# Kernel optimization log

Hardware: AMD Instinct MI355X
Metric: run time of the kernel (lower is better)

Reference implementation:

```python
import jax, jax.numpy as jnp
import numpy as np

DIM, D_STATE, D_CONV, EXPAND = 384, 16, 4, 2
D_INNER = EXPAND * DIM          # 768
DT_RANK = -(-DIM // 16)         # 24
B_, T_, H_, W_ = 2, 8, 16, 16
EPS = 1e-5


def layernorm(x, w, b):
    mu = x.mean(-1, keepdims=True)
    var = ((x - mu) ** 2).mean(-1, keepdims=True)
    return (x - mu) * jax.lax.rsqrt(var + EPS) * w + b


def setup_inputs() -> dict:
    key = jax.random.key(0)
    ks = jax.random.split(key, 12)
    std = 0.02
    x = jax.random.normal(ks[0], (B_, DIM, T_, H_, W_), jnp.float32)
    params = dict(
        ln1_w=jnp.ones((DIM,), jnp.float32),
        ln1_b=jnp.zeros((DIM,), jnp.float32),
        ln2_w=jnp.ones((DIM,), jnp.float32),
        ln2_b=jnp.zeros((DIM,), jnp.float32),
        in_proj_w=std * jax.random.normal(ks[1], (2 * D_INNER, DIM), jnp.float32),
        conv_w=std * jax.random.normal(ks[2], (D_INNER, 1, D_CONV), jnp.float32),
        conv_b=jnp.zeros((D_INNER,), jnp.float32),
        x_proj_w=std * jax.random.normal(ks[3], (DT_RANK + 2 * D_STATE, D_INNER), jnp.float32),
        dt_proj_w=std * jax.random.normal(ks[4], (D_INNER, DT_RANK), jnp.float32),
        dt_proj_b=0.01 * jax.random.normal(ks[5], (D_INNER,), jnp.float32),
        A_log=jnp.log(jnp.broadcast_to(jnp.arange(1, D_STATE + 1, dtype=jnp.float32), (D_INNER, D_STATE))),
        D=jnp.ones((D_INNER,), jnp.float32),
        out_proj_w=std * jax.random.normal(ks[6], (DIM, D_INNER), jnp.float32),
    )
    return {"x": x, **params}


def mamba(xn, in_proj_w, conv_w, conv_b, x_proj_w, dt_proj_w, dt_proj_b, A_log, D, out_proj_w):
    # xn: [B, L, dim]
    B, L, _ = xn.shape
    xz = xn @ in_proj_w.T                      # [B, L, 2*d_inner]
    u, z = jnp.split(xz, 2, axis=-1)
    # causal depthwise conv over tokens
    uc = jnp.transpose(u, (0, 2, 1))           # [B, d_inner, L]
    uc = jax.lax.conv_general_dilated(
        uc, conv_w, window_strides=(1,), padding=[(D_CONV - 1, 0)],
        dimension_numbers=("NCH", "OIH", "NCH"), feature_group_count=D_INNER)
    u = jax.nn.silu(jnp.transpose(uc, (0, 2, 1)) + conv_b)  # [B, L, d_inner]

    dbc = u @ x_proj_w.T                       # [B, L, dt_rank + 2*d_state]
    dt = dbc[..., :DT_RANK]
    Bm = dbc[..., DT_RANK:DT_RANK + D_STATE]   # [B, L, d_state]
    Cm = dbc[..., DT_RANK + D_STATE:]          # [B, L, d_state]
    delta = jax.nn.softplus(dt @ dt_proj_w.T + dt_proj_b)   # [B, L, d_inner]

    A = -jnp.exp(A_log)                        # [d_inner, d_state]
    deltaA = jnp.exp(delta[..., None] * A)                     # [B, L, d_inner, d_state]
    deltaBu = delta[..., None] * Bm[:, :, None, :] * u[..., None]

    def step(h, inp):
        dA, dBu, c = inp                       # [B,d_inner,d_state], [B,d_inner,d_state], [B,d_state]
        h = dA * h + dBu
        y = jnp.einsum("bds,bs->bd", h, c)
        return h, y

    h0 = jnp.zeros((B, D_INNER, D_STATE), xn.dtype)
    xs = (jnp.moveaxis(deltaA, 1, 0), jnp.moveaxis(deltaBu, 1, 0), jnp.moveaxis(Cm, 1, 0))
    _, ys = jax.lax.scan(step, h0, xs)
    y = jnp.moveaxis(ys, 0, 1)                 # [B, L, d_inner]
    y = y + u * D
    y = y * jax.nn.silu(z)
    return y @ out_proj_w.T                    # [B, L, dim]


def reference(x, ln1_w, ln1_b, ln2_w, ln2_b, in_proj_w, conv_w, conv_b,
              x_proj_w, dt_proj_w, dt_proj_b, A_log, D, out_proj_w):
    B, C, T, H, W = x.shape
    L = T * H * W
    x_flat = jnp.transpose(x.reshape(B, C, L), (0, 2, 1))   # [B, L, C]
    x_norm = layernorm(x_flat, ln1_w, ln1_b)
    x_mamba = mamba(x_norm, in_proj_w, conv_w, conv_b, x_proj_w,
                    dt_proj_w, dt_proj_b, A_log, D, out_proj_w)
    x_out = layernorm(x_flat + x_mamba, ln2_w, ln2_b)
    return jnp.transpose(x_out, (0, 2, 1)).reshape(B, C, T, H, W)
```

## Files before the change

### kernel.cpp

```cpp
#include <hip/hip_runtime.h>
#include <hip/hip_bf16.h>

typedef unsigned short u16;
typedef unsigned int   u32;
typedef __attribute__((ext_vector_type(8))) short short8;
typedef __attribute__((ext_vector_type(4))) float f32x4;

#define B_   2
#define L_   2048
#define CDIM 384
#define DI   768
#define DXZ  1536
#define DTR  24
#define DS   16
#define NDBC 56
#define NC   64
#define TC   32
#define TL   32
#define EPSV 1e-5f

#define OFFW_WIN  0
#define OFFW_WXP  589824
#define OFFW_WOUT 632832
#define TOTW      927744

__device__ __forceinline__ float bf2f(u16 u) {
    union { u32 i; float f; } v; v.i = ((u32)u) << 16; return v.f;
}
__device__ __forceinline__ u16 f2bf(float f) {
    union { float f; u32 i; } v; v.f = f;
    u32 x = v.i;
    u32 r = (x + 0x7FFFu + ((x >> 16) & 1u)) >> 16;
    return (u16)r;
}

__global__ __launch_bounds__(256) void ln1_convert(const float* __restrict__ x,
                                                   const float* __restrict__ w,
                                                   const float* __restrict__ bb,
                                                   u16* __restrict__ xn,
                                                   const float* __restrict__ win,
                                                   const float* __restrict__ wxp,
                                                   const float* __restrict__ wout,
                                                   u16* __restrict__ wdst) {
    __shared__ float tile[CDIM][TL + 1];
    __shared__ float red_s[8][TL];
    __shared__ float red_s2[8][TL];
    __shared__ float mu_s[TL], rs_s[TL];
    int tid = threadIdx.x, blk = blockIdx.x;
    if (blk >= 128) {
        int base = (blk - 128) * 256 + tid;
        for (int e = base; e < TOTW; e += 128 * 256) {
            float v;
            if (e < OFFW_WXP)       v = win[e];
            else if (e < OFFW_WOUT) v = wxp[e - OFFW_WXP];
            else                    v = wout[e - OFFW_WOUT];
            wdst[e] = f2bf(v);
        }
        return;
    }
    int b = blk >> 6;
    int l0 = (blk & 63) * TL;
    int cg = tid >> 5, li = tid & 31;
    const float* xp = x + (size_t)b * CDIM * L_ + l0 + li;
    float s = 0.f, s2 = 0.f;
#pragma unroll
    for (int c = cg; c < CDIM; c += 8) {
        float v = xp[(size_t)c * L_];
        tile[c][li] = v;
        s += v; s2 += v * v;
    }
    red_s[cg][li] = s; red_s2[cg][li] = s2;
    __syncthreads();
    if (tid < TL) {
        float ts = 0.f, ts2 = 0.f;
#pragma unroll
        for (int g = 0; g < 8; g++) { ts += red_s[g][tid]; ts2 += red_s2[g][tid]; }
        float mu = ts / CDIM;
        float var = ts2 / CDIM - mu * mu;
        mu_s[tid] = mu; rs_s[tid] = rsqrtf(var + EPSV);
    }
    __syncthreads();
    int wv = tid >> 6, lane = tid & 63;
#pragma unroll
    for (int r = 0; r < 8; r++) {
        int l = wv * 8 + r;
        float mu = mu_s[l], rs = rs_s[l];
        u16* op = xn + (size_t)(b * L_ + l0 + l) * CDIM;
#pragma unroll
        for (int j = 0; j < 6; j++) {
            int c = lane + 64 * j;
            float t = (tile[c][l] - mu) * rs * w[c] + bb[c];
            op[c] = f2bf(t);
        }
    }
}

template<int KN>
__global__ __launch_bounds__(256) void gemm_in(const u16* __restrict__ A,
                                               const u16* __restrict__ Bm,
                                               u16* __restrict__ Cp, int Nn) {
    int wave = threadIdx.x >> 6, lane = threadIdx.x & 63;
    int wm = wave & 1, wn = wave >> 1;
    int m0 = (blockIdx.x * 2 + wm) * 64;
    int n0 = (blockIdx.y * 2 + wn) * 64;
    int r = lane & 15, q = lane >> 4;
    f32x4 acc[4][4];
#pragma unroll
    for (int i = 0; i < 4; i++)
#pragma unroll
        for (int j = 0; j < 4; j++)
#pragma unroll
            for (int g = 0; g < 4; g++) acc[i][j][g] = 0.f;
#pragma unroll
    for (int k0 = 0; k0 < KN; k0 += 32) {
        short8 af[4], bf[4];
        int ka = k0 + q * 8;
#pragma unroll
        for (int i = 0; i < 4; i++) {
            af[i] = *(const short8*)(A + (size_t)(m0 + i * 16 + r) * KN + ka);
            bf[i] = *(const short8*)(Bm + (size_t)(n0 + i * 16 + r) * KN + ka);
        }
#pragma unroll
        for (int i = 0; i < 4; i++)
#pragma unroll
            for (int j = 0; j < 4; j++)
                acc[i][j] = __builtin_amdgcn_mfma_f32_16x16x32_bf16(af[i], bf[j], acc[i][j], 0, 0, 0);
    }
#pragma unroll
    for (int i = 0; i < 4; i++)
#pragma unroll
        for (int j = 0; j < 4; j++) {
            int col = n0 + j * 16 + r;
#pragma unroll
            for (int g = 0; g < 4; g++)
                Cp[(size_t)(m0 + i * 16 + q * 4 + g) * Nn + col] = f2bf(acc[i][j][g]);
        }
}

template<int KN, int NN>
__global__ __launch_bounds__(256) void gemm_out(const u16* __restrict__ A,
                                                const u16* __restrict__ Bm,
                                                float* __restrict__ Cp) {
    __shared__ float sm[2][64][66];
    int lane = threadIdx.x & 63, wave = threadIdx.x >> 6;
    int m0 = blockIdx.x * 64, n0 = blockIdx.y * 64;
    int r = lane & 15, q = lane >> 4;
    f32x4 acc[4][4];
#pragma unroll
    for (int i = 0; i < 4; i++)
#pragma unroll
        for (int j = 0; j < 4; j++)
#pragma unroll
            for (int g = 0; g < 4; g++) acc[i][j][g] = 0.f;
    const int KQ = KN / 4;
    int kb = wave * KQ;
#pragma unroll
    for (int k0 = 0; k0 < KQ; k0 += 32) {
        short8 af[4], bf[4];
        int ka = kb + k0 + q * 8;
#pragma unroll
        for (int i = 0; i < 4; i++) {
            af[i] = *(const short8*)(A + (size_t)(m0 + i * 16 + r) * KN + ka);
            bf[i] = *(const short8*)(Bm + (size_t)(n0 + i * 16 + r) * KN + ka);
        }
#pragma unroll
        for (int i = 0; i < 4; i++)
#pragma unroll
            for (int j = 0; j < 4; j++)
                acc[i][j] = __builtin_amdgcn_mfma_f32_16x16x32_bf16(af[i], bf[j], acc[i][j], 0, 0, 0);
    }
    if (wave < 2) {
#pragma unroll
        for (int i = 0; i < 4; i++)
#pragma unroll
            for (int j = 0; j < 4; j++)
#pragma unroll
                for (int g = 0; g < 4; g++)
                    sm[wave][i * 16 + q * 4 + g][j * 16 + r] = acc[i][j][g];
    }
    __syncthreads();
    if (wave >= 2) {
        int w2 = wave - 2;
#pragma unroll
        for (int i = 0; i < 4; i++)
#pragma unroll
            for (int j = 0; j < 4; j++)
#pragma unroll
                for (int g = 0; g < 4; g++)
                    sm[w2][i * 16 + q * 4 + g][j * 16 + r] += acc[i][j][g];
    }
    __syncthreads();
    for (int e = threadIdx.x; e < 64 * 64; e += 256) {
        int row = e >> 6, col = e & 63;
        Cp[(size_t)(m0 + row) * NN + n0 + col] = sm[0][row][col] + sm[1][row][col];
    }
}

template<int KN>
__global__ __launch_bounds__(256) void gemm_xp(const u16* __restrict__ A,
                                               const u16* __restrict__ Bm,
                                               float* __restrict__ Cp) {
    __shared__ float sm[2][16][66];
    int lane = threadIdx.x & 63, wave = threadIdx.x >> 6;
    int m0 = blockIdx.x * 16;
    int r = lane & 15, q = lane >> 4;
    f32x4 acc[4];
#pragma unroll
    for (int j = 0; j < 4; j++)
#pragma unroll
        for (int g = 0; g < 4; g++) acc[j][g] = 0.f;
    short8 zf;
#pragma unroll
    for (int e = 0; e < 8; e++) zf[e] = 0;
    const int KQ = KN / 4;
    int kb = wave * KQ;
#pragma unroll
    for (int k0 = 0; k0 < KQ; k0 += 32) {
        int ka = kb + k0 + q * 8;
        short8 af = *(const short8*)(A + (size_t)(m0 + r) * KN + ka);
        short8 bf[4];
#pragma unroll
        for (int j = 0; j < 4; j++) {
            int n = j * 16 + r;
            bf[j] = (n < NDBC) ? *(const short8*)(Bm + (size_t)n * KN + ka) : zf;
        }
#pragma unroll
        for (int j = 0; j < 4; j++)
            acc[j] = __builtin_amdgcn_mfma_f32_16x16x32_bf16(af, bf[j], acc[j], 0, 0, 0);
    }
    if (wave < 2) {
#pragma unroll
        for (int j = 0; j < 4; j++)
#pragma unroll
            for (int g = 0; g < 4; g++)
                sm[wave][q * 4 + g][j * 16 + r] = acc[j][g];
    }
    __syncthreads();
    if (wave >= 2) {
        int w2 = wave - 2;
#pragma unroll
        for (int j = 0; j < 4; j++)
#pragma unroll
            for (int g = 0; g < 4; g++)
                sm[w2][q * 4 + g][j * 16 + r] += acc[j][g];
    }
    __syncthreads();
    for (int e = threadIdx.x; e < 16 * 64; e += 256) {
        int row = e >> 6, col = e & 63;
        if (col < NDBC) {
            Cp[(size_t)(m0 + row) * NDBC + col] = sm[0][row][col] + sm[1][row][col];
        }
    }
}

__global__ __launch_bounds__(256) void conv_silu(const u16* __restrict__ xz,
                                                 const float* __restrict__ cw,
                                                 const float* __restrict__ cb,
                                                 u16* __restrict__ ubf) {
    int d = blockIdx.y * 256 + threadIdx.x;
    int m0 = blockIdx.x * 16;
    int l0 = m0 & (L_ - 1);
    float4 c4 = ((const float4*)cw)[d];
    float bias = cb[d];
    float w0, w1, w2;
    if (l0 == 0) { w0 = w1 = w2 = 0.f; }
    else {
        w0 = bf2f(xz[(size_t)(m0 - 3) * DXZ + d]);
        w1 = bf2f(xz[(size_t)(m0 - 2) * DXZ + d]);
        w2 = bf2f(xz[(size_t)(m0 - 1) * DXZ + d]);
    }
#pragma unroll
    for (int i = 0; i < 16; i++) {
        int m = m0 + i;
        float cur = bf2f(xz[(size_t)m * DXZ + d]);
        float acc = bias + w0 * c4.x + w1 * c4.y + w2 * c4.z + cur * c4.w;
        float sg = 1.f / (1.f + __expf(-acc));
        ubf[(size_t)m * DI + d] = f2bf(acc * sg);
        w0 = w1; w1 = w2; w2 = cur;
    }
}

__global__ __launch_bounds__(256) void scan_pass1(const u16* __restrict__ ubf,
                                                  const float* __restrict__ dbc,
                                                  const float* __restrict__ alogf,
                                                  const float* __restrict__ wdtf,
                                                  const float* __restrict__ bdtf,
                                                  float* __restrict__ chA,
                                                  float* __restrict__ chB) {
    int bc = blockIdx.x;
    int b = bc >> 6, chunk = bc & 63;
    int d = blockIdx.y * 256 + threadIdx.x;
    float a[DS], ap[DS], bv[DS], wdt[DTR];
#pragma unroll
    for (int s = 0; s < DS; s++) { a[s] = -__expf(alogf[d * DS + s]); ap[s] = 1.f; bv[s] = 0.f; }
#pragma unroll
    for (int k = 0; k < DTR; k++) wdt[k] = wdtf[d * DTR + k];
    float bd = bdtf[d];
    int t0 = b * L_ + chunk * TC;
#pragma unroll 2
    for (int t = t0; t < t0 + TC; t++) {
        const float* row = dbc + (size_t)t * NDBC;
        float acc = bd;
#pragma unroll
        for (int k = 0; k < DTR; k++) acc += row[k] * wdt[k];
        float dd = (acc > 20.f) ? acc : __logf(1.f + __expf(acc));
        float du = dd * bf2f(ubf[(size_t)t * DI + d]);
#pragma unroll
        for (int s = 0; s < DS; s++) {
            float dA = __expf(dd * a[s]);
            bv[s] = dA * bv[s] + du * row[DTR + s];
            ap[s] *= dA;
        }
    }
    float* pa = chA + (size_t)bc * DS * DI + d;
    float* pb = chB + (size_t)bc * DS * DI + d;
#pragma unroll
    for (int s = 0; s < DS; s++) { pa[(size_t)s * DI] = ap[s]; pb[(size_t)s * DI] = bv[s]; }
}

__global__ __launch_bounds__(256) void scan_mid(const float* __restrict__ chA,
                                                const float* __restrict__ chB,
                                                float* __restrict__ hin) {
    int idx = blockIdx.x * 256 + threadIdx.x;
    int b = idx / (DI * DS);
    int rem = idx - b * (DI * DS);
    float h = 0.f;
#pragma unroll 4
    for (int c = 0; c < NC; c++) {
        size_t off = ((size_t)(b * NC + c) * DI) * DS + rem;
        hin[off] = h;
        h = chA[off] * h + chB[off];
    }
}

__global__ __launch_bounds__(256) void scan_pass2(const u16* __restrict__ ubf,
                                                  const float* __restrict__ dbc,
                                                  const float* __restrict__ alogf,
                                                  const float* __restrict__ wdtf,
                                                  const float* __restrict__ bdtf,
                                                  const float* __restrict__ hin,
                                                  const float* __restrict__ Dwf,
                                                  const u16* __restrict__ xz,
                                                  u16* __restrict__ ym) {
    int bc = blockIdx.x;
    int b = bc >> 6, chunk = bc & 63;
    int d = blockIdx.y * 256 + threadIdx.x;
    float a[DS], h[DS], wdt[DTR];
#pragma unroll
    for (int s = 0; s < DS; s++) a[s] = -__expf(alogf[d * DS + s]);
#pragma unroll
    for (int k = 0; k < DTR; k++) wdt[k] = wdtf[d * DTR + k];
    float bd = bdtf[d];
    const float* hp = hin + (size_t)bc * DS * DI + d;
#pragma unroll
    for (int s = 0; s < DS; s++) h[s] = hp[(size_t)s * DI];
    float dD = Dwf[d];
    int t0 = b * L_ + chunk * TC;
#pragma unroll 2
    for (int t = t0; t < t0 + TC; t++) {
        const float* row = dbc + (size_t)t * NDBC;
        float acc = bd;
#pragma unroll
        for (int k = 0; k < DTR; k++) acc += row[k] * wdt[k];
        float dd = (acc > 20.f) ? acc : __logf(1.f + __expf(acc));
        float uu = bf2f(ubf[(size_t)t * DI + d]);
        float du = dd * uu;
        float y = 0.f;
#pragma unroll
        for (int s = 0; s < DS; s++) {
            float dA = __expf(dd * a[s]);
            h[s] = dA * h[s] + du * row[DTR + s];
            y += h[s] * row[DTR + DS + s];
        }
        float z = bf2f(xz[(size_t)t * DXZ + DI + d]);
        float sg = 1.f / (1.f + __expf(-z));
        ym[(size_t)t * DI + d] = f2bf((y + uu * dD) * (z * sg));
    }
}

__global__ __launch_bounds__(256) void ln2_out(const float* __restrict__ x,
                                               const float* __restrict__ om,
                                               const float* __restrict__ w,
                                               const float* __restrict__ bb,
                                               float* __restrict__ out) {
    __shared__ float tile[CDIM][TL + 1];
    __shared__ float mu_s[TL], rs_s[TL];
    int tid = threadIdx.x, blk = blockIdx.x;
    int b = blk >> 6;
    int l0 = (blk & 63) * TL;
    int cg = tid >> 5, li = tid & 31;
    const float* xp = x + (size_t)b * CDIM * L_ + l0 + li;
#pragma unroll
    for (int c = cg; c < CDIM; c += 8) tile[c][li] = xp[(size_t)c * L_];
    __syncthreads();
    int wv = tid >> 6, lane = tid & 63;
#pragma unroll
    for (int r = 0; r < 8; r++) {
        int l = wv * 8 + r;
        const float* op = om + (size_t)(b * L_ + l0 + l) * CDIM;
        float s = 0.f, s2 = 0.f;
#pragma unroll
        for (int j = 0; j < 6; j++) {
            int c = lane + 64 * j;
            float t = tile[c][l] + op[c];
            tile[c][l] = t;
            s += t; s2 += t * t;
        }
#pragma unroll
        for (int off = 32; off > 0; off >>= 1) { s += __shfl_xor(s, off); s2 += __shfl_xor(s2, off); }
        if (lane == 0) {
            float mu = s / CDIM;
            float var = s2 / CDIM - mu * mu;
            mu_s[l] = mu; rs_s[l] = rsqrtf(var + EPSV);
        }
    }
    __syncthreads();
    float* outp = out + (size_t)b * CDIM * L_ + l0 + li;
    float mu = mu_s[li], rs = rs_s[li];
#pragma unroll
    for (int c = cg; c < CDIM; c += 8) {
        float t = (tile[c][li] - mu) * rs * w[c] + bb[c];
        outp[(size_t)c * L_] = t;
    }
}

extern "C" void kernel_launch(void* const* d_in, const int* in_sizes, int n_in,
                              void* d_out, int out_size, void* d_ws, size_t ws_size,
                              hipStream_t stream) {
    const float* x    = (const float*)d_in[0];
    const float* ln1w = (const float*)d_in[1];
    const float* ln1b = (const float*)d_in[2];
    const float* ln2w = (const float*)d_in[3];
    const float* ln2b = (const float*)d_in[4];
    const float* win  = (const float*)d_in[5];
    const float* cw   = (const float*)d_in[6];
    const float* cb   = (const float*)d_in[7];
    const float* wxp  = (const float*)d_in[8];
    const float* wdt  = (const float*)d_in[9];
    const float* bdt  = (const float*)d_in[10];
    const float* alog = (const float*)d_in[11];
    const float* Dw   = (const float*)d_in[12];
    const float* wout = (const float*)d_in[13];

    char* ws = (char*)d_ws;
    u16*   wbf   = (u16*)(ws + 0);
    u16*   win_b  = wbf + OFFW_WIN;
    u16*   wxp_b  = wbf + OFFW_WXP;
    u16*   wout_b = wbf + OFFW_WOUT;
    u16*   xn    = (u16*)(ws + 1855488);
    u16*   xz    = (u16*)(ws + 5001216);
    u16*   ubf   = (u16*)(ws + 17584128);
    float* dbc   = (float*)(ws + 23875584);
    float* chA   = (float*)(ws + 24793088);
    float* chB   = (float*)(ws + 31084544);
    float* hin   = (float*)(ws + 37376000);
    u16*   ym    = (u16*)(ws + 43667456);
    float* om    = (float*)(ws + 49958912);

    ln1_convert<<<dim3(256), 256, 0, stream>>>(x, ln1w, ln1b, xn, win, wxp, wout, wbf);
    gemm_in<384><<<dim3(32, 12), 256, 0, stream>>>(xn, win_b, xz, DXZ);
    conv_silu<<<dim3(256, 3), 256, 0, stream>>>(xz, cw, cb, ubf);
    gemm_xp<768><<<dim3(256), 256, 0, stream>>>(ubf, wxp_b, dbc);
    scan_pass1<<<dim3(128, 3), 256, 0, stream>>>(ubf, dbc, alog, wdt, bdt, chA, chB);
    scan_mid<<<96, 256, 0, stream>>>(chA, chB, hin);
    scan_pass2<<<dim3(128, 3), 256, 0, stream>>>(ubf, dbc, alog, wdt, bdt, hin, Dw, xz, ym);
    gemm_out<768, 384><<<dim3(64, 6), 256, 0, stream>>>(ym, wout_b, om);
    ln2_out<<<dim3(128), 256, 0, stream>>>(x, om, ln2w, ln2b, (float*)d_out);
}
```

Baseline: 219.7 us.

## Fuse all stages into one persistent kernel with grid-wide atomic barriers

Replaces the nine separate kernel launches with one persistent 256-block, 512-thread kernel. The stages (LN1, in-proj GEMM, conv, x-proj, scan passes, out-proj, LN2) are separated by software grid barriers built on atomics and sleep loops, with a memset to reset the barrier counters. The goal is to remove per-launch overhead and gaps between kernels. In exchange the kernel relies on all 256 blocks being co-resident to avoid deadlock, some stages now run on fewer blocks or with different work splits, and it adds barrier spin cost.

```diff
diff --git a/kernel.cpp b/kernel.cpp
--- a/kernel.cpp
+++ b/kernel.cpp
@@ -24,6 +24,9 @@
 #define OFFW_WOUT 632832
 #define TOTW      927744
 
+#define NBLK 256
+#define NTHR 512
+
 __device__ __forceinline__ float bf2f(u16 u) {
     union { u32 i; float f; } v; v.i = ((u32)u) << 16; return v.f;
 }
@@ -34,393 +37,400 @@
     return (u16)r;
 }
 
-__global__ __launch_bounds__(256) void ln1_convert(const float* __restrict__ x,
-                                                   const float* __restrict__ w,
-                                                   const float* __restrict__ bb,
-                                                   u16* __restrict__ xn,
-                                                   const float* __restrict__ win,
-                                                   const float* __restrict__ wxp,
-                                                   const float* __restrict__ wout,
-                                                   u16* __restrict__ wdst) {
-    __shared__ float tile[CDIM][TL + 1];
-    __shared__ float red_s[8][TL];
-    __shared__ float red_s2[8][TL];
-    __shared__ float mu_s[TL], rs_s[TL];
+__device__ __forceinline__ void gbar(int* bar, int slot) {
+    __syncthreads();
+    if (threadIdx.x == 0) {
+        int* p = bar + slot * 64;
+        __threadfence();
+        __hip_atomic_fetch_add(p, 1, __ATOMIC_RELEASE, __HIP_MEMORY_SCOPE_AGENT);
+        while (__hip_atomic_load(p, __ATOMIC_ACQUIRE, __HIP_MEMORY_SCOPE_AGENT) < NBLK)
+            __builtin_amdgcn_s_sleep(8);
+        __threadfence();
+    }
+    __syncthreads();
+}
+
+struct P0S { float tile[CDIM][TL + 1]; float red[16][TL]; float red2[16][TL]; float mu[TL]; float rs[TL]; };
+struct P3S { float sm[4][16][66]; };
+struct P7S { float sm[4][64][64]; };
+struct P8S { float tile[CDIM][TL + 1]; float mu[TL]; float rs[TL]; };
+
+__global__ __launch_bounds__(NTHR, 2) void mega(
+    const float* x, const float* ln1w, const float* ln1b,
+    const float* ln2w, const float* ln2b,
+    const float* win, const float* cw, const float* cb,
+    const float* wxp, const float* wdt, const float* bdt,
+    const float* alog, const float* Dw, const float* wout,
+    u16* wbf, u16* xn, u16* xz, u16* ubf,
+    float* dbc, float* chA, float* chB, float* hin,
+    u16* ym, float* om, float* out, int* bar)
+{
+    __shared__ __align__(16) char smem[65536];
     int tid = threadIdx.x, blk = blockIdx.x;
-    if (blk >= 128) {
-        int base = (blk - 128) * 256 + tid;
-        for (int e = base; e < TOTW; e += 128 * 256) {
+
+    if (blk < 128) {
+        P0S& S = *(P0S*)smem;
+        int b = blk >> 6, l0 = (blk & 63) * TL;
+        int cg = tid >> 5, li = tid & 31;
+        const float* xp = x + (size_t)b * CDIM * L_ + l0 + li;
+        float s = 0.f, s2 = 0.f;
+#pragma unroll
+        for (int c = cg; c < CDIM; c += 16) {
+            float v = xp[(size_t)c * L_];
+            S.tile[c][li] = v;
+            s += v; s2 += v * v;
+        }
+        S.red[cg][li] = s; S.red2[cg][li] = s2;
+        __syncthreads();
+        if (tid < TL) {
+            float ts = 0.f, ts2 = 0.f;
+#pragma unroll
+            for (int g = 0; g < 16; g++) { ts += S.red[g][tid]; ts2 += S.red2[g][tid]; }
+            float mu = ts / CDIM;
+            float var = ts2 / CDIM - mu * mu;
+            S.mu[tid] = mu; S.rs[tid] = rsqrtf(var + EPSV);
+        }
+        __syncthreads();
+        int wv = tid >> 6, lane = tid & 63;
+#pragma unroll
+        for (int r = 0; r < 4; r++) {
+            int l = wv * 4 + r;
+            float mu = S.mu[l], rs = S.rs[l];
+            u16* op = xn + (size_t)(b * L_ + l0 + l) * CDIM;
+#pragma unroll
+            for (int j = 0; j < 6; j++) {
+                int c = lane + 64 * j;
+                float t = (S.tile[c][l] - mu) * rs * ln1w[c] + ln1b[c];
+                op[c] = f2bf(t);
+            }
+        }
+    } else {
+        int base = (blk - 128) * NTHR + tid;
+        for (int e = base; e < TOTW; e += 128 * NTHR) {
             float v;
             if (e < OFFW_WXP)       v = win[e];
             else if (e < OFFW_WOUT) v = wxp[e - OFFW_WXP];
             else                    v = wout[e - OFFW_WOUT];
-            wdst[e] = f2bf(v);
-        }
-        return;
-    }
-    int b = blk >> 6;
-    int l0 = (blk & 63) * TL;
-    int cg = tid >> 5, li = tid & 31;
-    const float* xp = x + (size_t)b * CDIM * L_ + l0 + li;
-    float s = 0.f, s2 = 0.f;
-#pragma unroll
-    for (int c = cg; c < CDIM; c += 8) {
-        float v = xp[(size_t)c * L_];
-        tile[c][li] = v;
-        s += v; s2 += v * v;
-    }
-    red_s[cg][li] = s; red_s2[cg][li] = s2;
-    __syncthreads();
-    if (tid < TL) {
-        float ts = 0.f, ts2 = 0.f;
-#pragma unroll
-        for (int g = 0; g < 8; g++) { ts += red_s[g][tid]; ts2 += red_s2[g][tid]; }
-        float mu = ts / CDIM;
-        float var = ts2 / CDIM - mu * mu;
-        mu_s[tid] = mu; rs_s[tid] = rsqrtf(var + EPSV);
-    }
-    __syncthreads();
-    int wv = tid >> 6, lane = tid & 63;
-#pragma unroll
-    for (int r = 0; r < 8; r++) {
-        int l = wv * 8 + r;
-        float mu = mu_s[l], rs = rs_s[l];
-        u16* op = xn + (size_t)(b * L_ + l0 + l) * CDIM;
-#pragma unroll
-        for (int j = 0; j < 6; j++) {
-            int c = lane + 64 * j;
-            float t = (tile[c][l] - mu) * rs * w[c] + bb[c];
-            op[c] = f2bf(t);
-        }
-    }
-}
-
-template<int KN>
-__global__ __launch_bounds__(256) void gemm_in(const u16* __restrict__ A,
-                                               const u16* __restrict__ Bm,
-                                               u16* __restrict__ Cp, int Nn) {
-    int wave = threadIdx.x >> 6, lane = threadIdx.x & 63;
-    int wm = wave & 1, wn = wave >> 1;
-    int m0 = (blockIdx.x * 2 + wm) * 64;
-    int n0 = (blockIdx.y * 2 + wn) * 64;
-    int r = lane & 15, q = lane >> 4;
-    f32x4 acc[4][4];
-#pragma unroll
-    for (int i = 0; i < 4; i++)
+            wbf[e] = f2bf(v);
+        }
+    }
+    gbar(bar, 0);
+
+    if (blk < 192) {
+        int wave = tid >> 6, lane = tid & 63;
+        int wm = wave & 1, wn = wave >> 1;
+        int bx = blk & 31, by = blk >> 5;
+        int m0 = (bx * 2 + wm) * 64;
+        int n0 = (by * 4 + wn) * 64;
+        int r = lane & 15, q = lane >> 4;
+        const u16* Bw = wbf + OFFW_WIN;
+        f32x4 acc[4][4];
+#pragma unroll
+        for (int i = 0; i < 4; i++)
+#pragma unroll
+            for (int j = 0; j < 4; j++)
+#pragma unroll
+                for (int g = 0; g < 4; g++) acc[i][j][g] = 0.f;
+#pragma unroll
+        for (int k0 = 0; k0 < CDIM; k0 += 32) {
+            short8 af[4], bfv[4];
+            int ka = k0 + q * 8;
+#pragma unroll
+            for (int i = 0; i < 4; i++) {
+                af[i]  = *(const short8*)(xn + (size_t)(m0 + i * 16 + r) * CDIM + ka);
+                bfv[i] = *(const short8*)(Bw + (size_t)(n0 + i * 16 + r) * CDIM + ka);
+            }
+#pragma unroll
+            for (int i = 0; i < 4; i++)
+#pragma unroll
+                for (int j = 0; j < 4; j++)
+                    acc[i][j] = __builtin_amdgcn_mfma_f32_16x16x32_bf16(af[i], bfv[j], acc[i][j], 0, 0, 0);
+        }
+#pragma unroll
+        for (int i = 0; i < 4; i++)
+#pragma unroll
+            for (int j = 0; j < 4; j++) {
+                int col = n0 + j * 16 + r;
+#pragma unroll
+                for (int g = 0; g < 4; g++)
+                    xz[(size_t)(m0 + i * 16 + q * 4 + g) * DXZ + col] = f2bf(acc[i][j][g]);
+            }
+    }
+    gbar(bar, 1);
+
+    {
+#pragma unroll
+        for (int it = 0; it < 2; it++) {
+            int g = it * (NBLK * NTHR) + blk * NTHR + tid;
+            if (g < 768 * 256) {
+                int d = g % DI;
+                int m0 = (g / DI) * 16;
+                int l0 = m0 & (L_ - 1);
+                float4 c4 = ((const float4*)cw)[d];
+                float bias = cb[d];
+                float w0, w1, w2;
+                if (l0 == 0) { w0 = w1 = w2 = 0.f; }
+                else {
+                    w0 = bf2f(xz[(size_t)(m0 - 3) * DXZ + d]);
+                    w1 = bf2f(xz[(size_t)(m0 - 2) * DXZ + d]);
+                    w2 = bf2f(xz[(size_t)(m0 - 1) * DXZ + d]);
+                }
+#pragma unroll
+                for (int i = 0; i < 16; i++) {
+                    int m = m0 + i;
+                    float cur = bf2f(xz[(size_t)m * DXZ + d]);
+                    float acc = bias + w0 * c4.x + w1 * c4.y + w2 * c4.z + cur * c4.w;
+                    float sg = 1.f / (1.f + __expf(-acc));
+                    ubf[(size_t)m * DI + d] = f2bf(acc * sg);
+                    w0 = w1; w1 = w2; w2 = cur;
+                }
+            }
+        }
+    }
+    gbar(bar, 2);
+
+    {
+        P3S& S = *(P3S*)smem;
+        int wave = tid >> 6, lane = tid & 63;
+        int m0 = blk * 16;
+        int r = lane & 15, q = lane >> 4;
+        const u16* Bw = wbf + OFFW_WXP;
+        f32x4 acc[4];
 #pragma unroll
         for (int j = 0; j < 4; j++)
 #pragma unroll
-            for (int g = 0; g < 4; g++) acc[i][j][g] = 0.f;
-#pragma unroll
-    for (int k0 = 0; k0 < KN; k0 += 32) {
-        short8 af[4], bf[4];
-        int ka = k0 + q * 8;
-#pragma unroll
-        for (int i = 0; i < 4; i++) {
-            af[i] = *(const short8*)(A + (size_t)(m0 + i * 16 + r) * KN + ka);
-            bf[i] = *(const short8*)(Bm + (size_t)(n0 + i * 16 + r) * KN + ka);
-        }
-#pragma unroll
-        for (int i = 0; i < 4; i++)
+            for (int g = 0; g < 4; g++) acc[j][g] = 0.f;
+        short8 zf;
+#pragma unroll
+        for (int e = 0; e < 8; e++) zf[e] = 0;
+        int kb = wave * 96;
+#pragma unroll
+        for (int k0 = 0; k0 < 96; k0 += 32) {
+            int ka = kb + k0 + q * 8;
+            short8 af = *(const short8*)(ubf + (size_t)(m0 + r) * DI + ka);
+            short8 bfv[4];
+#pragma unroll
+            for (int j = 0; j < 4; j++) {
+                int n = j * 16 + r;
+                bfv[j] = (n < NDBC) ? *(const short8*)(Bw + (size_t)n * DI + ka) : zf;
+            }
 #pragma unroll
             for (int j = 0; j < 4; j++)
-                acc[i][j] = __builtin_amdgcn_mfma_f32_16x16x32_bf16(af[i], bf[j], acc[i][j], 0, 0, 0);
-    }
-#pragma unroll
-    for (int i = 0; i < 4; i++)
-#pragma unroll
-        for (int j = 0; j < 4; j++) {
-            int col = n0 + j * 16 + r;
-#pragma unroll
-            for (int g = 0; g < 4; g++)
-                Cp[(size_t)(m0 + i * 16 + q * 4 + g) * Nn + col] = f2bf(acc[i][j][g]);
-        }
-}
-
-template<int KN, int NN>
-__global__ __launch_bounds__(256) void gemm_out(const u16* __restrict__ A,
-                                                const u16* __restrict__ Bm,
-                                                float* __restrict__ Cp) {
-    __shared__ float sm[2][64][66];
-    int lane = threadIdx.x & 63, wave = threadIdx.x >> 6;
-    int m0 = blockIdx.x * 64, n0 = blockIdx.y * 64;
-    int r = lane & 15, q = lane >> 4;
-    f32x4 acc[4][4];
-#pragma unroll
-    for (int i = 0; i < 4; i++)
-#pragma unroll
-        for (int j = 0; j < 4; j++)
-#pragma unroll
-            for (int g = 0; g < 4; g++) acc[i][j][g] = 0.f;
-    const int KQ = KN / 4;
-    int kb = wave * KQ;
-#pragma unroll
-    for (int k0 = 0; k0 < KQ; k0 += 32) {
-        short8 af[4], bf[4];
-        int ka = kb + k0 + q * 8;
-#pragma unroll
-        for (int i = 0; i < 4; i++) {
-            af[i] = *(const short8*)(A + (size_t)(m0 + i * 16 + r) * KN + ka);
-            bf[i] = *(const short8*)(Bm + (size_t)(n0 + i * 16 + r) * KN + ka);
-        }
-#pragma unroll
-        for (int i = 0; i < 4; i++)
+                acc[j] = __builtin_amdgcn_mfma_f32_16x16x32_bf16(af, bfv[j], acc[j], 0, 0, 0);
+        }
+        if (wave < 4) {
 #pragma unroll
             for (int j = 0; j < 4; j++)
-                acc[i][j] = __builtin_amdgcn_mfma_f32_16x16x32_bf16(af[i], bf[j], acc[i][j], 0, 0, 0);
-    }
-    if (wave < 2) {
-#pragma unroll
-        for (int i = 0; i < 4; i++)
+#pragma unroll
+                for (int g = 0; g < 4; g++)
+                    S.sm[wave][q * 4 + g][j * 16 + r] = acc[j][g];
+        }
+        __syncthreads();
+        if (wave >= 4) {
 #pragma unroll
             for (int j = 0; j < 4; j++)
 #pragma unroll
                 for (int g = 0; g < 4; g++)
-                    sm[wave][i * 16 + q * 4 + g][j * 16 + r] = acc[i][j][g];
-    }
-    __syncthreads();
-    if (wave >= 2) {
-        int w2 = wave - 2;
-#pragma unroll
-        for (int i = 0; i < 4; i++)
-#pragma unroll
-            for (int j = 0; j < 4; j++)
-#pragma unroll
-                for (int g = 0; g < 4; g++)
-                    sm[w2][i * 16 + q * 4 + g][j * 16 + r] += acc[i][j][g];
-    }
-    __syncthreads();
-    for (int e = threadIdx.x; e < 64 * 64; e += 256) {
-        int row = e >> 6, col = e & 63;
-        Cp[(size_t)(m0 + row) * NN + n0 + col] = sm[0][row][col] + sm[1][row][col];
-    }
-}
-
-template<int KN>
-__global__ __launch_bounds__(256) void gemm_xp(const u16* __restrict__ A,
-                                               const u16* __restrict__ Bm,
-                                               float* __restrict__ Cp) {
-    __shared__ float sm[2][16][66];
-    int lane = threadIdx.x & 63, wave = threadIdx.x >> 6;
-    int m0 = blockIdx.x * 16;
-    int r = lane & 15, q = lane >> 4;
-    f32x4 acc[4];
-#pragma unroll
-    for (int j = 0; j < 4; j++)
-#pragma unroll
-        for (int g = 0; g < 4; g++) acc[j][g] = 0.f;
-    short8 zf;
-#pragma unroll
-    for (int e = 0; e < 8; e++) zf[e] = 0;
-    const int KQ = KN / 4;
-    int kb = wave * KQ;
-#pragma unroll
-    for (int k0 = 0; k0 < KQ; k0 += 32) {
-        int ka = kb + k0 + q * 8;
-        short8 af = *(const short8*)(A + (size_t)(m0 + r) * KN + ka);
-        short8 bf[4];
-#pragma unroll
-        for (int j = 0; j < 4; j++) {
-            int n = j * 16 + r;
-            bf[j] = (n < NDBC) ? *(const short8*)(Bm + (size_t)n * KN + ka) : zf;
-        }
-#pragma unroll
-        for (int j = 0; j < 4; j++)
-            acc[j] = __builtin_amdgcn_mfma_f32_16x16x32_bf16(af, bf[j], acc[j], 0, 0, 0);
-    }
-    if (wave < 2) {
-#pragma unroll
-        for (int j = 0; j < 4; j++)
-#pragma unroll
-            for (int g = 0; g < 4; g++)
-                sm[wave][q * 4 + g][j * 16 + r] = acc[j][g];
-    }
-    __syncthreads();
-    if (wave >= 2) {
-        int w2 = wave - 2;
-#pragma unroll
-        for (int j = 0; j < 4; j++)
-#pragma unroll
-            for (int g = 0; g < 4; g++)
-                sm[w2][q * 4 + g][j * 16 + r] += acc[j][g];
-    }
-    __syncthreads();
-    for (int e = threadIdx.x; e < 16 * 64; e += 256) {
-        int row = e >> 6, col = e & 63;
-        if (col < NDBC) {
-            Cp[(size_t)(m0 + row) * NDBC + col] = sm[0][row][col] + sm[1][row][col];
-        }
-    }
-}
-
-__global__ __launch_bounds__(256) void conv_silu(const u16* __restrict__ xz,
-                                                 const float* __restrict__ cw,
-                                                 const float* __restrict__ cb,
-                                                 u16* __restrict__ ubf) {
-    int d = blockIdx.y * 256 + threadIdx.x;
-    int m0 = blockIdx.x * 16;
-    int l0 = m0 & (L_ - 1);
-    float4 c4 = ((const float4*)cw)[d];
-    float bias = cb[d];
-    float w0, w1, w2;
-    if (l0 == 0) { w0 = w1 = w2 = 0.f; }
-    else {
-        w0 = bf2f(xz[(size_t)(m0 - 3) * DXZ + d]);
-        w1 = bf2f(xz[(size_t)(m0 - 2) * DXZ + d]);
-        w2 = bf2f(xz[(size_t)(m0 - 1) * DXZ + d]);
-    }
-#pragma unroll
-    for (int i = 0; i < 16; i++) {
-        int m = m0 + i;
-        float cur = bf2f(xz[(size_t)m * DXZ + d]);
-        float acc = bias + w0 * c4.x + w1 * c4.y + w2 * c4.z + cur * c4.w;
-        float sg = 1.f / (1.f + __expf(-acc));
-        ubf[(size_t)m * DI + d] = f2bf(acc * sg);
-        w0 = w1; w1 = w2; w2 = cur;
-    }
-}
-
-__global__ __launch_bounds__(256) void scan_pass1(const u16* __restrict__ ubf,
-                                                  const float* __restrict__ dbc,
-                                                  const float* __restrict__ alogf,
-                                                  const float* __restrict__ wdtf,
-                                                  const float* __restrict__ bdtf,
-                                                  float* __restrict__ chA,
-                                                  float* __restrict__ chB) {
-    int bc = blockIdx.x;
-    int b = bc >> 6, chunk = bc & 63;
-    int d = blockIdx.y * 256 + threadIdx.x;
-    float a[DS], ap[DS], bv[DS], wdt[DTR];
-#pragma unroll
-    for (int s = 0; s < DS; s++) { a[s] = -__expf(alogf[d * DS + s]); ap[s] = 1.f; bv[s] = 0.f; }
-#pragma unroll
-    for (int k = 0; k < DTR; k++) wdt[k] = wdtf[d * DTR + k];
-    float bd = bdtf[d];
-    int t0 = b * L_ + chunk * TC;
+                    S.sm[wave - 4][q * 4 + g][j * 16 + r] += acc[j][g];
+        }
+        __syncthreads();
+        for (int e = tid; e < 16 * 64; e += NTHR) {
+            int row = e >> 6, col = e & 63;
+            if (col < NDBC)
+                dbc[(size_t)(m0 + row) * NDBC + col] =
+                    S.sm[0][row][col] + S.sm[1][row][col] + S.sm[2][row][col] + S.sm[3][row][col];
+        }
+    }
+    gbar(bar, 3);
+
+    {
+        int g = blk * NTHR + tid;
+        if (g < 128 * DI) {
+            int d = g % DI, bc = g / DI;
+            int b = bc >> 6, chunk = bc & 63;
+            float a[DS], ap[DS], bv[DS], wdtv[DTR];
+#pragma unroll
+            for (int s = 0; s < DS; s++) { a[s] = -__expf(alog[d * DS + s]); ap[s] = 1.f; bv[s] = 0.f; }
+#pragma unroll
+            for (int k = 0; k < DTR; k++) wdtv[k] = wdt[d * DTR + k];
+            float bd = bdt[d];
+            int t0 = b * L_ + chunk * TC;
 #pragma unroll 2
-    for (int t = t0; t < t0 + TC; t++) {
-        const float* row = dbc + (size_t)t * NDBC;
-        float acc = bd;
-#pragma unroll
-        for (int k = 0; k < DTR; k++) acc += row[k] * wdt[k];
-        float dd = (acc > 20.f) ? acc : __logf(1.f + __expf(acc));
-        float du = dd * bf2f(ubf[(size_t)t * DI + d]);
-#pragma unroll
-        for (int s = 0; s < DS; s++) {
-            float dA = __expf(dd * a[s]);
-            bv[s] = dA * bv[s] + du * row[DTR + s];
-            ap[s] *= dA;
-        }
-    }
-    float* pa = chA + (size_t)bc * DS * DI + d;
-    float* pb = chB + (size_t)bc * DS * DI + d;
-#pragma unroll
-    for (int s = 0; s < DS; s++) { pa[(size_t)s * DI] = ap[s]; pb[(size_t)s * DI] = bv[s]; }
-}
-
-__global__ __launch_bounds__(256) void scan_mid(const float* __restrict__ chA,
-                                                const float* __restrict__ chB,
-                                                float* __restrict__ hin) {
-    int idx = blockIdx.x * 256 + threadIdx.x;
-    int b = idx / (DI * DS);
-    int rem = idx - b * (DI * DS);
-    float h = 0.f;
+            for (int t = t0; t < t0 + TC; t++) {
+                const float* row = dbc + (size_t)t * NDBC;
+                float acc = bd;
+#pragma unroll
+                for (int k = 0; k < DTR; k++) acc += row[k] * wdtv[k];
+                float dd = (acc > 20.f) ? acc : __logf(1.f + __expf(acc));
+                float du = dd * bf2f(ubf[(size_t)t * DI + d]);
+#pragma unroll
+                for (int s = 0; s < DS; s++) {
+                    float dA = __expf(dd * a[s]);
+                    bv[s] = dA * bv[s] + du * row[DTR + s];
+                    ap[s] *= dA;
+                }
+            }
+            float* pa = chA + (size_t)bc * DS * DI + d;
+            float* pb = chB + (size_t)bc * DS * DI + d;
+#pragma unroll
+            for (int s = 0; s < DS; s++) { pa[(size_t)s * DI] = ap[s]; pb[(size_t)s * DI] = bv[s]; }
+        }
+    }
+    gbar(bar, 4);
+
+    {
+        int idx = blk * NTHR + tid;
+        if (idx < B_ * DI * DS) {
+            int b = idx / (DI * DS);
+            int rem = idx - b * (DI * DS);
+            float h = 0.f;
 #pragma unroll 4
-    for (int c = 0; c < NC; c++) {
-        size_t off = ((size_t)(b * NC + c) * DI) * DS + rem;
-        hin[off] = h;
-        h = chA[off] * h + chB[off];
-    }
-}
-
-__global__ __launch_bounds__(256) void scan_pass2(const u16* __restrict__ ubf,
-                                                  const float* __restrict__ dbc,
-                                                  const float* __restrict__ alogf,
-                                                  const float* __restrict__ wdtf,
-                                                  const float* __restrict__ bdtf,
-                                                  const float* __restrict__ hin,
-                                                  const float* __restrict__ Dwf,
-                                                  const u16* __restrict__ xz,
-                                                  u16* __restrict__ ym) {
-    int bc = blockIdx.x;
-    int b = bc >> 6, chunk = bc & 63;
-    int d = blockIdx.y * 256 + threadIdx.x;
-    float a[DS], h[DS], wdt[DTR];
-#pragma unroll
-    for (int s = 0; s < DS; s++) a[s] = -__expf(alogf[d * DS + s]);
-#pragma unroll
-    for (int k = 0; k < DTR; k++) wdt[k] = wdtf[d * DTR + k];
-    float bd = bdtf[d];
-    const float* hp = hin + (size_t)bc * DS * DI + d;
-#pragma unroll
-    for (int s = 0; s < DS; s++) h[s] = hp[(size_t)s * DI];
-    float dD = Dwf[d];
-    int t0 = b * L_ + chunk * TC;
+            for (int c = 0; c < NC; c++) {
+                size_t off = ((size_t)(b * NC + c) * DI) * DS + rem;
+                hin[off] = h;
+                h = chA[off] * h + chB[off];
+            }
+        }
+    }
+    gbar(bar, 5);
+
+    {
+        int g = blk * NTHR + tid;
+        if (g < 128 * DI) {
+            int d = g % DI, bc = g / DI;
+            int b = bc >> 6, chunk = bc & 63;
+            float a[DS], h[DS], wdtv[DTR];
+#pragma unroll
+            for (int s = 0; s < DS; s++) a[s] = -__expf(alog[d * DS + s]);
+#pragma unroll
+            for (int k = 0; k < DTR; k++) wdtv[k] = wdt[d * DTR + k];
+            float bd = bdt[d];
+            const float* hp = hin + (size_t)bc * DS * DI + d;
+#pragma unroll
+            for (int s = 0; s < DS; s++) h[s] = hp[(size_t)s * DI];
+            float dD = Dw[d];
+            int t0 = b * L_ + chunk * TC;
 #pragma unroll 2
-    for (int t = t0; t < t0 + TC; t++) {
-        const float* row = dbc + (size_t)t * NDBC;
-        float acc = bd;
-#pragma unroll
-        for (int k = 0; k < DTR; k++) acc += row[k] * wdt[k];
-        float dd = (acc > 20.f) ? acc : __logf(1.f + __expf(acc));
-        float uu = bf2f(ubf[(size_t)t * DI + d]);
-        float du = dd * uu;
-        float y = 0.f;
-#pragma unroll
-        for (int s = 0; s < DS; s++) {
-            float dA = __expf(dd * a[s]);
-            h[s] = dA * h[s] + du * row[DTR + s];
-            y += h[s] * row[DTR + DS + s];
-        }
-        float z = bf2f(xz[(size_t)t * DXZ + DI + d]);
-        float sg = 1.f / (1.f + __expf(-z));
-        ym[(size_t)t * DI + d] = f2bf((y + uu * dD) * (z * sg));
-    }
-}
-
-__global__ __launch_bounds__(256) void ln2_out(const float* __restrict__ x,
-                                               const float* __restrict__ om,
-                                               const float* __restrict__ w,
-                                               const float* __restrict__ bb,
-                                               float* __restrict__ out) {
-    __shared__ float tile[CDIM][TL + 1];
-    __shared__ float mu_s[TL], rs_s[TL];
-    int tid = threadIdx.x, blk = blockIdx.x;
-    int b = blk >> 6;
-    int l0 = (blk & 63) * TL;
-    int cg = tid >> 5, li = tid & 31;
-    const float* xp = x + (size_t)b * CDIM * L_ + l0 + li;
-#pragma unroll
-    for (int c = cg; c < CDIM; c += 8) tile[c][li] = xp[(size_t)c * L_];
-    __syncthreads();
-    int wv = tid >> 6, lane = tid & 63;
-#pragma unroll
-    for (int r = 0; r < 8; r++) {
-        int l = wv * 8 + r;
-        const float* op = om + (size_t)(b * L_ + l0 + l) * CDIM;
-        float s = 0.f, s2 = 0.f;
-#pragma unroll
-        for (int j = 0; j < 6; j++) {
-            int c = lane + 64 * j;
-            float t = tile[c][l] + op[c];
-            tile[c][l] = t;
-            s += t; s2 += t * t;
-        }
-#pragma unroll
-        for (int off = 32; off > 0; off >>= 1) { s += __shfl_xor(s, off); s2 += __shfl_xor(s2, off); }
-        if (lane == 0) {
-            float mu = s / CDIM;
-            float var = s2 / CDIM - mu * mu;
-            mu_s[l] = mu; rs_s[l] = rsqrtf(var + EPSV);
-        }
-    }
-    __syncthreads();
-    float* outp = out + (size_t)b * CDIM * L_ + l0 + li;
-    float mu = mu_s[li], rs = rs_s[li];
-#pragma unroll
-    for (int c = cg; c < CDIM; c += 8) {
-        float t = (tile[c][li] - mu) * rs * w[c] + bb[c];
-        outp[(size_t)c * L_] = t;
+            for (int t = t0; t < t0 + TC; t++) {
+                const float* row = dbc + (size_t)t * NDBC;
+                float acc = bd;
+#pragma unroll
+                for (int k = 0; k < DTR; k++) acc += row[k] * wdtv[k];
+                float dd = (acc > 20.f) ? acc : __logf(1.f + __expf(acc));
+                float uu = bf2f(ubf[(size_t)t * DI + d]);
+                float du = dd * uu;
+                float y = 0.f;
+#pragma unroll
+                for (int s = 0; s < DS; s++) {
+                    float dA = __expf(dd * a[s]);
+                    h[s] = dA * h[s] + du * row[DTR + s];
+                    y += h[s] * row[DTR + DS + s];
+                }
+                float z = bf2f(xz[(size_t)t * DXZ + DI + d]);
+                float sg = 1.f / (1.f + __expf(-z));
+                ym[(size_t)t * DI + d] = f2bf((y + uu * dD) * (z * sg));
+            }
+        }
+    }
+    gbar(bar, 6);
+
+    {
+        P7S& S = *(P7S*)smem;
+        int wave = tid >> 6, lane = tid & 63;
+        int r = lane & 15, q = lane >> 4;
+        const u16* Bw = wbf + OFFW_WOUT;
+        for (int t = blk; t < 384; t += NBLK) {
+            int m0 = (t & 63) * 64, n0 = (t >> 6) * 64;
+            f32x4 acc[4][4];
+#pragma unroll
+            for (int i = 0; i < 4; i++)
+#pragma unroll
+                for (int j = 0; j < 4; j++)
+#pragma unroll
+                    for (int g = 0; g < 4; g++) acc[i][j][g] = 0.f;
+            int kb = wave * 96;
+#pragma unroll
+            for (int k0 = 0; k0 < 96; k0 += 32) {
+                short8 af[4], bfv[4];
+                int ka = kb + k0 + q * 8;
+#pragma unroll
+                for (int i = 0; i < 4; i++) {
+                    af[i]  = *(const short8*)(ym + (size_t)(m0 + i * 16 + r) * DI + ka);
+                    bfv[i] = *(const short8*)(Bw + (size_t)(n0 + i * 16 + r) * DI + ka);
+                }
+#pragma unroll
+                for (int i = 0; i < 4; i++)
+#pragma unroll
+                    for (int j = 0; j < 4; j++)
+                        acc[i][j] = __builtin_amdgcn_mfma_f32_16x16x32_bf16(af[i], bfv[j], acc[i][j], 0, 0, 0);
+            }
+            if (wave < 4) {
+#pragma unroll
+                for (int i = 0; i < 4; i++)
+#pragma unroll
+                    for (int j = 0; j < 4; j++)
+#pragma unroll
+                        for (int g = 0; g < 4; g++)
+                            S.sm[wave][i * 16 + q * 4 + g][j * 16 + r] = acc[i][j][g];
+            }
+            __syncthreads();
+            if (wave >= 4) {
+#pragma unroll
+                for (int i = 0; i < 4; i++)
+#pragma unroll
+                    for (int j = 0; j < 4; j++)
+#pragma unroll
+                        for (int g = 0; g < 4; g++)
+                            S.sm[wave - 4][i * 16 + q * 4 + g][j * 16 + r] += acc[i][j][g];
+            }
+            __syncthreads();
+            for (int e = tid; e < 64 * 64; e += NTHR) {
+                int row = e >> 6, col = e & 63;
+                om[(size_t)(m0 + row) * CDIM + n0 + col] =
+                    S.sm[0][row][col] + S.sm[1][row][col] + S.sm[2][row][col] + S.sm[3][row][col];
+            }
+            __syncthreads();
+        }
+    }
+    gbar(bar, 7);
+
+    if (blk < 128) {
+        P8S& S = *(P8S*)smem;
+        int b = blk >> 6, l0 = (blk & 63) * TL;
+        int cg = tid >> 5, li = tid & 31;
+        const float* xp = x + (size_t)b * CDIM * L_ + l0 + li;
+#pragma unroll
+        for (int c = cg; c < CDIM; c += 16) S.tile[c][li] = xp[(size_t)c * L_];
+        __syncthreads();
+        int wv = tid >> 6, lane = tid & 63;
+#pragma unroll
+        for (int r = 0; r < 4; r++) {
+            int l = wv * 4 + r;
+            const float* op = om + (size_t)(b * L_ + l0 + l) * CDIM;
+            float s = 0.f, s2 = 0.f;
+#pragma unroll
+            for (int j = 0; j < 6; j++) {
+                int c = lane + 64 * j;
+                float t = S.tile[c][l] + op[c];
+                S.tile[c][l] = t;
+                s += t; s2 += t * t;
+            }
+#pragma unroll
+            for (int off = 32; off > 0; off >>= 1) { s += __shfl_xor(s, off); s2 += __shfl_xor(s2, off); }
+            if (lane == 0) {
+                float mu = s / CDIM;
+                float var = s2 / CDIM - mu * mu;
+                S.mu[l] = mu; S.rs[l] = rsqrtf(var + EPSV);
+            }
+        }
+        __syncthreads();
+        float* outp = out + (size_t)b * CDIM * L_ + l0 + li;
+        float mu = S.mu[li], rs = S.rs[li];
+#pragma unroll
+        for (int c = cg; c < CDIM; c += 16) {
+            float t = (S.tile[c][li] - mu) * rs * ln2w[c] + ln2b[c];
+            outp[(size_t)c * L_] = t;
+        }
     }
 }
 
@@ -443,27 +453,21 @@
     const float* wout = (const float*)d_in[13];
 
     char* ws = (char*)d_ws;
-    u16*   wbf   = (u16*)(ws + 0);
-    u16*   win_b  = wbf + OFFW_WIN;
-    u16*   wxp_b  = wbf + OFFW_WXP;
-    u16*   wout_b = wbf + OFFW_WOUT;
-    u16*   xn    = (u16*)(ws + 1855488);
-    u16*   xz    = (u16*)(ws + 5001216);
-    u16*   ubf   = (u16*)(ws + 17584128);
-    float* dbc   = (float*)(ws + 23875584);
-    float* chA   = (float*)(ws + 24793088);
-    float* chB   = (float*)(ws + 31084544);
-    float* hin   = (float*)(ws + 37376000);
-    u16*   ym    = (u16*)(ws + 43667456);
-    float* om    = (float*)(ws + 49958912);
-
-    ln1_convert<<<dim3(256), 256, 0, stream>>>(x, ln1w, ln1b, xn, win, wxp, wout, wbf);
-    gemm_in<384><<<dim3(32, 12), 256, 0, stream>>>(xn, win_b, xz, DXZ);
-    conv_silu<<<dim3(256, 3), 256, 0, stream>>>(xz, cw, cb, ubf);
-    gemm_xp<768><<<dim3(256), 256, 0, stream>>>(ubf, wxp_b, dbc);
-    scan_pass1<<<dim3(128, 3), 256, 0, stream>>>(ubf, dbc, alog, wdt, bdt, chA, chB);
-    scan_mid<<<96, 256, 0, stream>>>(chA, chB, hin);
-    scan_pass2<<<dim3(128, 3), 256, 0, stream>>>(ubf, dbc, alog, wdt, bdt, hin, Dw, xz, ym);
-    gemm_out<768, 384><<<dim3(64, 6), 256, 0, stream>>>(ym, wout_b, om);
-    ln2_out<<<dim3(128), 256, 0, stream>>>(x, om, ln2w, ln2b, (float*)d_out);
+    u16*   wbf  = (u16*)(ws + 0);
+    u16*   xn   = (u16*)(ws + 1855488);
+    u16*   xz   = (u16*)(ws + 5001216);
+    u16*   ubf  = (u16*)(ws + 17584128);
+    float* dbc  = (float*)(ws + 23875584);
+    float* chA  = (float*)(ws + 24793088);
+    float* chB  = (float*)(ws + 31084544);
+    float* hin  = (float*)(ws + 37376000);
+    u16*   ym   = (u16*)(ws + 43667456);
+    float* om   = (float*)(ws + 49958912);
+    int*   bar  = (int*)(ws + 56623104);
+
+    hipMemsetAsync(bar, 0, 4096, stream);
+    mega<<<NBLK, NTHR, 0, stream>>>(x, ln1w, ln1b, ln2w, ln2b, win, cw, cb,
+                                    wxp, wdt, bdt, alog, Dw, wout,
+                                    wbf, xn, xz, ubf, dbc, chA, chB, hin,
+                                    ym, om, (float*)d_out, bar);
 }
```

Result: slower. 650.4 us (+196.0%).
